# Performance work log

Hardware: AMD Instinct MI355X
Metric: run time of the kernel (lower is better)

The kernel has to match this reference:

```python
import jax, jax.numpy as jnp
import numpy as np

N = 50000      # nodes
E = 1600000    # edges (avg degree 32)
DIN, DH, DOUT = 256, 128, 64


def gcn_conv(x, W, b, row, col, w, n):
    """One GCNConv layer (self-loops already appended to row/col/w).
    row = source nodes, col = target nodes; aggregate at targets."""
    xw = x @ W                                        # [n, d_out]
    deg = jax.ops.segment_sum(w, col, num_segments=n)  # in-degree weighted
    dinv = jnp.where(deg > 0, jax.lax.rsqrt(deg), 0.0)
    norm = dinv[row] * w * dinv[col]                  # [E+n]
    msg = norm[:, None] * xw[row]                     # [E+n, d_out] gather
    out = jax.ops.segment_sum(msg, col, num_segments=n)
    return out + b


def setup_inputs() -> dict:
    key = jax.random.key(0)
    k = jax.random.split(key, 6)
    x = jax.random.normal(k[0], (N, DIN), dtype=jnp.float32)
    edge_index = jax.random.randint(k[1], (2, E), 0, N)
    edge_weight = jax.random.uniform(k[2], (E,), dtype=jnp.float32)
    W1 = jax.random.normal(k[3], (DIN, DH), dtype=jnp.float32) * (1.0 / np.sqrt(DIN))
    b1 = jnp.zeros((DH,), dtype=jnp.float32)
    W2 = jax.random.normal(k[4], (DH, DOUT), dtype=jnp.float32) * (1.0 / np.sqrt(DH))
    b2 = jnp.zeros((DOUT,), dtype=jnp.float32)
    return {"x": x, "edge_index": edge_index, "edge_weight": edge_weight,
            "W1": W1, "b1": b1, "W2": W2, "b2": b2}


def reference(x, edge_index, edge_weight, W1, b1, W2, b2):
    n = x.shape[0]
    loops = jnp.arange(n, dtype=edge_index.dtype)
    row = jnp.concatenate([edge_index[0], loops])
    col = jnp.concatenate([edge_index[1], loops])
    w = jnp.concatenate([edge_weight, jnp.ones((n,), dtype=edge_weight.dtype)])
    h = gcn_conv(x, W1, b1, row, col, w, n)
    h = jax.nn.relu(h)
    # dropout(p=0.2) is identity in eval mode
    h = gcn_conv(h, W2, b2, row, col, w, n)
    return jax.nn.log_softmax(h, axis=-1)
```

## Files before the change

### kernel.cpp

```cpp
#include <hip/hip_runtime.h>
#include <hip/hip_bf16.h>
#include <cstddef>


#define DIN 256
#define DH  128
#define DOUT 64
#define NPB 100
#define NBMAX 512

typedef __bf16 bf16x8 __attribute__((ext_vector_type(8)));
typedef float f32x4 __attribute__((ext_vector_type(4)));

__device__ __forceinline__ float bflo(unsigned u) { return __uint_as_float(u << 16); }
__device__ __forceinline__ float bfhi(unsigned u) { return __uint_as_float(u & 0xffff0000u); }
__device__ __forceinline__ unsigned short f2bf(float f) {
    unsigned u = __float_as_uint(f);
    unsigned r = (u + 0x7fffu + ((u >> 16) & 1u)) >> 16;
    return (unsigned short)r;
}

__device__ __forceinline__ int2 ldrec(const int2* __restrict__ e, int idx, int last, int fb) {
    int ci = idx < last ? idx : last;
    int2 r = e[ci];
    if (idx > last) { r.x = fb; r.y = 0; }
    return r;
}

__global__ void prep_w_kernel(const float* __restrict__ W1, const float* __restrict__ W2,
                              unsigned short* __restrict__ wt1, unsigned short* __restrict__ wt2) {
    int i = blockIdx.x * 256 + threadIdx.x;
    if (i < DH * DIN) {
        int nn = i >> 8, k = i & 255;
        wt1[i] = f2bf(W1[k * DH + nn]);
    } else {
        int j = i - DH * DIN;
        if (j < DOUT * DH) {
            int nn = j >> 7, k = j & 127;
            wt2[j] = f2bf(W2[k * DOUT + nn]);
        }
    }
}

__launch_bounds__(256)
__global__ void hist_kernel(const int* __restrict__ col, int* __restrict__ bh,
                            int E, int Ec, int NB) {
    __shared__ int hist[NBMAX];
    int p = blockIdx.x, t = threadIdx.x;
    for (int b = t; b < NB; b += 256) hist[b] = 0;
    __syncthreads();
    int s = p * Ec, e = min(s + Ec, E);
    for (int i = s + t; i < e; i += 256) atomicAdd(&hist[col[i] / NPB], 1);
    __syncthreads();
    for (int b = t; b < NB; b += 256) bh[p * NB + b] = hist[b];
}

__launch_bounds__(512)
__global__ void colscan_kernel(int* __restrict__ bh, int* __restrict__ btotal,
                               int P, int NB) {
    __shared__ int arr[512];
    int b = blockIdx.x, t = threadIdx.x;
    arr[t] = (t < P) ? bh[t * NB + b] : 0;
    __syncthreads();
    for (int off = 1; off < 512; off <<= 1) {
        int v = (t >= off) ? arr[t - off] : 0;
        __syncthreads();
        arr[t] += v;
        __syncthreads();
    }
    int excl = (t == 0) ? 0 : arr[t - 1];
    if (t < P) bh[t * NB + b] = excl;
    if (t == P - 1) btotal[b] = arr[t];
}

__launch_bounds__(512)
__global__ void basescan_kernel(const int* __restrict__ btotal, int* __restrict__ bbase,
                                int* __restrict__ rowptr, int NB, int n, int E) {
    __shared__ int arr[512];
    int t = threadIdx.x;
    arr[t] = (t < NB) ? btotal[t] : 0;
    __syncthreads();
    for (int off = 1; off < 512; off <<= 1) {
        int v = (t >= off) ? arr[t - off] : 0;
        __syncthreads();
        arr[t] += v;
        __syncthreads();
    }
    int excl = (t == 0) ? 0 : arr[t - 1];
    if (t <= NB) bbase[t] = excl;
    if (t == 511) rowptr[n] = E;
}

__launch_bounds__(256)
__global__ void scatter_kernel(const int* __restrict__ row, const int* __restrict__ col,
                               const float* __restrict__ w, const int* __restrict__ bh,
                               const int* __restrict__ bbase, int2* __restrict__ part,
                               int E, int Ec, int NB) {
    __shared__ int cur[NBMAX];
    int p = blockIdx.x, t = threadIdx.x;
    for (int b = t; b < NB; b += 256) cur[b] = bbase[b] + bh[p * NB + b];
    __syncthreads();
    int s = p * Ec, e = min(s + Ec, E);
    for (int i = s + t; i < e; i += 256) {
        int c = col[i];
        int r = row[i];
        int b = c / NPB;
        int pos = atomicAdd(&cur[b], 1);
        part[pos] = make_int2(r | ((c - b * NPB) << 16), __float_as_int(w[i]));
    }
}

__launch_bounds__(256)
__global__ void bucket_csr_kernel(const int2* __restrict__ part, const int* __restrict__ bbase,
                                  float* __restrict__ dinv, int* __restrict__ rowptr,
                                  int2* __restrict__ final_e, int n) {
    __shared__ int   hist[NPB];
    __shared__ float wsum[NPB];
    __shared__ int   nbase[NPB];
    __shared__ int   cur[NPB];
    int b = blockIdx.x, t = threadIdx.x;
    if (t < NPB) { hist[t] = 0; wsum[t] = 0.0f; }
    __syncthreads();
    int s = bbase[b], e = bbase[b + 1];
    for (int i = s + t; i < e; i += 256) {
        int2 rec = part[i];
        int cl = rec.x >> 16;
        atomicAdd(&hist[cl], 1);
        atomicAdd(&wsum[cl], __int_as_float(rec.y));
    }
    __syncthreads();
    if (t == 0) {
        int run = 0;
        for (int k = 0; k < NPB; ++k) { nbase[k] = run; run += hist[k]; }
    }
    __syncthreads();
    if (t < NPB) {
        int node = b * NPB + t;
        if (node < n) {
            dinv[node] = rsqrtf(1.0f + wsum[t]);
            rowptr[node] = s + nbase[t];
        }
        cur[t] = nbase[t];
    }
    __syncthreads();
    for (int i = s + t; i < e; i += 256) {
        int2 rec = part[i];
        int cl = rec.x >> 16;
        int q = s + atomicAdd(&cur[cl], 1);
        final_e[q] = make_int2(rec.x & 0xffff, rec.y);
    }
}

template <int K, int M>
__launch_bounds__(256)
__global__ void gemm_mfma_kernel(const float* __restrict__ A,
                                 const unsigned short* __restrict__ Wt,
                                 const float* __restrict__ scale,
                                 unsigned short* __restrict__ C, int N) {
    constexpr int BK = 64, LD = BK + 8;
    constexpr int WN = M / 4;
    constexpr int NT = WN / 16;
    constexpr int CLD = M + 8;
    constexpr int SM = (64 * LD + M * LD) > (64 * CLD) ? (64 * LD + M * LD) : (64 * CLD);
    __shared__ unsigned short smem[SM];
    __shared__ float sdv[64];
    unsigned short* As = smem;
    unsigned short* Bs = smem + 64 * LD;

    const int tid = threadIdx.x;
    const int row0 = blockIdx.x * 64;
    const int lane = tid & 63;
    const int quad = lane >> 4, r16 = lane & 15;
    const int n0 = (tid >> 6) * WN;

    if (tid < 64) {
        int r = row0 + tid;
        sdv[tid] = (r < N) ? scale[r] : 0.0f;
    }

    f32x4 acc[4][NT];
#pragma unroll
    for (int mt = 0; mt < 4; ++mt)
#pragma unroll
        for (int nt = 0; nt < NT; ++nt)
            acc[mt][nt] = (f32x4){0.f, 0.f, 0.f, 0.f};

    for (int k0 = 0; k0 < K; k0 += BK) {
#pragma unroll
        for (int j = 0; j < 4; ++j) {
            int idx = tid + j * 256;
            int m = idx >> 4;
            int q = idx & 15;
            int gr = row0 + m;
            float4 v = make_float4(0.f, 0.f, 0.f, 0.f);
            if (gr < N) v = *(const float4*)&A[(size_t)gr * K + k0 + q * 4];
            ushort4 s4;
            s4.x = f2bf(v.x); s4.y = f2bf(v.y); s4.z = f2bf(v.z); s4.w = f2bf(v.w);
            *(ushort4*)&As[m * LD + q * 4] = s4;
        }
#pragma unroll
        for (int j = 0; j < M * 8 / 256; ++j) {
            int idx = tid + j * 256;
            int nn = idx >> 3;
            int q = idx & 7;
            uint4 v = *(const uint4*)&Wt[(size_t)nn * K + k0 + q * 8];
            *(uint4*)&Bs[nn * LD + q * 8] = v;
        }
        __syncthreads();
#pragma unroll
        for (int ks = 0; ks < BK / 32; ++ks) {
            bf16x8 af[4], bfr[NT];
#pragma unroll
            for (int nt = 0; nt < NT; ++nt)
                bfr[nt] = *(const bf16x8*)&Bs[(n0 + nt * 16 + r16) * LD + ks * 32 + quad * 8];
#pragma unroll
            for (int mt = 0; mt < 4; ++mt)
                af[mt] = *(const bf16x8*)&As[(mt * 16 + r16) * LD + ks * 32 + quad * 8];
#pragma unroll
            for (int mt = 0; mt < 4; ++mt)
#pragma unroll
                for (int nt = 0; nt < NT; ++nt)
                    acc[mt][nt] = __builtin_amdgcn_mfma_f32_16x16x32_bf16(
                        af[mt], bfr[nt], acc[mt][nt], 0, 0, 0);
        }
        __syncthreads();
    }
    unsigned short* Cs = smem;
#pragma unroll
    for (int mt = 0; mt < 4; ++mt) {
#pragma unroll
        for (int i = 0; i < 4; ++i) {
            int r = mt * 16 + quad * 4 + i;
            float sc = sdv[r];
#pragma unroll
            for (int nt = 0; nt < NT; ++nt)
                Cs[r * CLD + n0 + nt * 16 + r16] = f2bf(acc[mt][nt][i] * sc);
        }
    }
    __syncthreads();
#pragma unroll
    for (int j = 0; j < 64 * M / 8 / 256; ++j) {
        int idx = tid + j * 256;
        int r = idx / (M / 8);
        int q = idx % (M / 8);
        int gr = row0 + r;
        if (gr < N) {
            uint4 v = *(const uint4*)&Cs[r * CLD + q * 8];
            *(uint4*)&C[(size_t)gr * M + q * 8] = v;
        }
    }
}

#define ACC8(v, wgt)                                            \
    a0 += (wgt) * bflo((v).x); a1 += (wgt) * bfhi((v).x);       \
    a2 += (wgt) * bflo((v).y); a3 += (wgt) * bfhi((v).y);       \
    a4 += (wgt) * bflo((v).z); a5 += (wgt) * bfhi((v).z);       \
    a6 += (wgt) * bflo((v).w); a7 += (wgt) * bfhi((v).w);

__launch_bounds__(256, 8)
__global__ void agg1_kernel(const unsigned short* __restrict__ xw,
                            const int* __restrict__ rowptr,
                            const int2* __restrict__ edge,
                            const float* __restrict__ dinv,
                            const float* __restrict__ bias,
                            float* __restrict__ out, int n) {
    int node = blockIdx.x * 4 + (threadIdx.x >> 6);
    if (node >= n) return;
    int lane = threadIdx.x & 63;
    int qw = lane >> 4, sub = lane & 15;
    const char* xb = (const char*)xw;
    const unsigned ssub = (unsigned)sub << 4;
    float di = dinv[node];

    float a0 = 0.f, a1 = 0.f, a2 = 0.f, a3 = 0.f;
    float a4 = 0.f, a5 = 0.f, a6 = 0.f, a7 = 0.f;
    if (qw == 0) {
        uint4 u = *(const uint4*)(xb + (((unsigned)node) << 8) + ssub);
        a0 = bflo(u.x); a1 = bfhi(u.x); a2 = bflo(u.y); a3 = bfhi(u.y);
        a4 = bflo(u.z); a5 = bfhi(u.z); a6 = bflo(u.w); a7 = bfhi(u.w);
    }

    int p = rowptr[node], p1 = rowptr[node + 1];
    int sbase = 4 * qw;
    int2 ea, eb, ec, ed;
    bool have = (p + 16 <= p1);
    if (have) {
        const int2* rp = edge + p + sbase;
        ea = rp[0]; eb = rp[1]; ec = rp[2]; ed = rp[3];
    }
#pragma unroll 1
    while (have) {
        uint4 v0 = *(const uint4*)(xb + (((unsigned)ea.x) << 8) + ssub);
        uint4 v1 = *(const uint4*)(xb + (((unsigned)eb.x) << 8) + ssub);
        uint4 v2 = *(const uint4*)(xb + (((unsigned)ec.x) << 8) + ssub);
        uint4 v3 = *(const uint4*)(xb + (((unsigned)ed.x) << 8) + ssub);
        float w0 = __int_as_float(ea.y), w1 = __int_as_float(eb.y);
        float w2 = __int_as_float(ec.y), w3 = __int_as_float(ed.y);
        p += 16;
        have = (p + 16 <= p1);
        if (have) {
            const int2* rp = edge + p + sbase;
            ea = rp[0]; eb = rp[1]; ec = rp[2]; ed = rp[3];
        }
        ACC8(v0, w0); ACC8(v1, w1); ACC8(v2, w2); ACC8(v3, w3);
    }
    int rem = p1 - p;
    if (rem > 0) {
        int last = p1 - 1, b2 = p + sbase;
        int2 e0 = ldrec(edge, b2, last, node);
        int2 e1 = ldrec(edge, b2 + 1, last, node);
        int2 e2 = ldrec(edge, b2 + 2, last, node);
        int2 e3 = ldrec(edge, b2 + 3, last, node);
        uint4 v0 = *(const uint4*)(xb + (((unsigned)e0.x) << 8) + ssub);
        uint4 v1 = *(const uint4*)(xb + (((unsigned)e1.x) << 8) + ssub);
        uint4 v2 = *(const uint4*)(xb + (((unsigned)e2.x) << 8) + ssub);
        uint4 v3 = *(const uint4*)(xb + (((unsigned)e3.x) << 8) + ssub);
        float w0 = __int_as_float(e0.y), w1 = __int_as_float(e1.y);
        float w2 = __int_as_float(e2.y), w3 = __int_as_float(e3.y);
        ACC8(v0, w0); ACC8(v1, w1); ACC8(v2, w2); ACC8(v3, w3);
    }
    a0 += __shfl_xor(a0, 16); a0 += __shfl_xor(a0, 32);
    a1 += __shfl_xor(a1, 16); a1 += __shfl_xor(a1, 32);
    a2 += __shfl_xor(a2, 16); a2 += __shfl_xor(a2, 32);
    a3 += __shfl_xor(a3, 16); a3 += __shfl_xor(a3, 32);
    a4 += __shfl_xor(a4, 16); a4 += __shfl_xor(a4, 32);
    a5 += __shfl_xor(a5, 16); a5 += __shfl_xor(a5, 32);
    a6 += __shfl_xor(a6, 16); a6 += __shfl_xor(a6, 32);
    a7 += __shfl_xor(a7, 16); a7 += __shfl_xor(a7, 32);
    if (qw < 2) {
        float4 b = ((const float4*)bias)[2 * sub + qw];
        float4 o = (qw == 0) ? make_float4(a0, a1, a2, a3)
                             : make_float4(a4, a5, a6, a7);
        o.x = fmaxf(di * o.x + b.x, 0.f);
        o.y = fmaxf(di * o.y + b.y, 0.f);
        o.z = fmaxf(di * o.z + b.z, 0.f);
        o.w = fmaxf(di * o.w + b.w, 0.f);
        ((float4*)out)[(size_t)node * 32 + 2 * sub + qw] = o;
    }
}

__launch_bounds__(256, 8)
__global__ void agg2_kernel(const unsigned short* __restrict__ xw,
                            const int* __restrict__ rowptr,
                            const int2* __restrict__ edge,
                            const float* __restrict__ dinv,
                            const float* __restrict__ bias,
                            float* __restrict__ out, int n) {
    int node = blockIdx.x * 4 + (threadIdx.x >> 6);
    if (node >= n) return;
    int lane = threadIdx.x & 63;
    int oct = lane >> 3, sub = lane & 7;
    const char* xb = (const char*)xw;
    const unsigned ssub = (unsigned)sub << 4;
    float di = dinv[node];

    float a0 = 0.f, a1 = 0.f, a2 = 0.f, a3 = 0.f;
    float a4 = 0.f, a5 = 0.f, a6 = 0.f, a7 = 0.f;
    if (oct == 0) {
        uint4 u = *(const uint4*)(xb + (((unsigned)node) << 7) + ssub);
        a0 = bflo(u.x); a1 = bfhi(u.x); a2 = bflo(u.y); a3 = bfhi(u.y);
        a4 = bflo(u.z); a5 = bfhi(u.z); a6 = bflo(u.w); a7 = bfhi(u.w);
    }

    int p = rowptr[node], p1 = rowptr[node + 1];
    int sbase = 4 * oct;
    int2 ea, eb, ec, ed;
    bool have = (p + 32 <= p1);
    if (have) {
        const int2* rp = edge + p + sbase;
        ea = rp[0]; eb = rp[1]; ec = rp[2]; ed = rp[3];
    }
#pragma unroll 1
    while (have) {
        uint4 v0 = *(const uint4*)(xb + (((unsigned)ea.x) << 7) + ssub);
        uint4 v1 = *(const uint4*)(xb + (((unsigned)eb.x) << 7) + ssub);
        uint4 v2 = *(const uint4*)(xb + (((unsigned)ec.x) << 7) + ssub);
        uint4 v3 = *(const uint4*)(xb + (((unsigned)ed.x) << 7) + ssub);
        float w0 = __int_as_float(ea.y), w1 = __int_as_float(eb.y);
        float w2 = __int_as_float(ec.y), w3 = __int_as_float(ed.y);
        p += 32;
        have = (p + 32 <= p1);
        if (have) {
            const int2* rp = edge + p + sbase;
            ea = rp[0]; eb = rp[1]; ec = rp[2]; ed = rp[3];
        }
        ACC8(v0, w0); ACC8(v1, w1); ACC8(v2, w2); ACC8(v3, w3);
    }
    int rem = p1 - p;
    if (rem > 0) {
        int last = p1 - 1, b2 = p + sbase;
        int2 e0 = ldrec(edge, b2, last, node);
        int2 e1 = ldrec(edge, b2 + 1, last, node);
        int2 e2 = ldrec(edge, b2 + 2, last, node);
        int2 e3 = ldrec(edge, b2 + 3, last, node);
        uint4 v0 = *(const uint4*)(xb + (((unsigned)e0.x) << 7) + ssub);
        uint4 v1 = *(const uint4*)(xb + (((unsigned)e1.x) << 7) + ssub);
        uint4 v2 = *(const uint4*)(xb + (((unsigned)e2.x) << 7) + ssub);
        uint4 v3 = *(const uint4*)(xb + (((unsigned)e3.x) << 7) + ssub);
        float w0 = __int_as_float(e0.y), w1 = __int_as_float(e1.y);
        float w2 = __int_as_float(e2.y), w3 = __int_as_float(e3.y);
        ACC8(v0, w0); ACC8(v1, w1); ACC8(v2, w2); ACC8(v3, w3);
    }
    a0 += __shfl_xor(a0, 8); a0 += __shfl_xor(a0, 16); a0 += __shfl_xor(a0, 32);
    a1 += __shfl_xor(a1, 8); a1 += __shfl_xor(a1, 16); a1 += __shfl_xor(a1, 32);
    a2 += __shfl_xor(a2, 8); a2 += __shfl_xor(a2, 16); a2 += __shfl_xor(a2, 32);
    a3 += __shfl_xor(a3, 8); a3 += __shfl_xor(a3, 16); a3 += __shfl_xor(a3, 32);
    a4 += __shfl_xor(a4, 8); a4 += __shfl_xor(a4, 16); a4 += __shfl_xor(a4, 32);
    a5 += __shfl_xor(a5, 8); a5 += __shfl_xor(a5, 16); a5 += __shfl_xor(a5, 32);
    a6 += __shfl_xor(a6, 8); a6 += __shfl_xor(a6, 16); a6 += __shfl_xor(a6, 32);
    a7 += __shfl_xor(a7, 8); a7 += __shfl_xor(a7, 16); a7 += __shfl_xor(a7, 32);
    const float4* bp = (const float4*)bias;
    float4 bl = bp[2 * sub], bh = bp[2 * sub + 1];
    a0 = di * a0 + bl.x; a1 = di * a1 + bl.y; a2 = di * a2 + bl.z; a3 = di * a3 + bl.w;
    a4 = di * a4 + bh.x; a5 = di * a5 + bh.y; a6 = di * a6 + bh.z; a7 = di * a7 + bh.w;
    float m = fmaxf(fmaxf(fmaxf(a0, a1), fmaxf(a2, a3)),
                    fmaxf(fmaxf(a4, a5), fmaxf(a6, a7)));
    m = fmaxf(m, __shfl_xor(m, 4));
    m = fmaxf(m, __shfl_xor(m, 2));
    m = fmaxf(m, __shfl_xor(m, 1));
    float s = __expf(a0 - m) + __expf(a1 - m) + __expf(a2 - m) + __expf(a3 - m)
            + __expf(a4 - m) + __expf(a5 - m) + __expf(a6 - m) + __expf(a7 - m);
    s += __shfl_xor(s, 4);
    s += __shfl_xor(s, 2);
    s += __shfl_xor(s, 1);
    float lse = m + __logf(s);
    if (oct < 2) {
        float4 o = (oct == 0) ? make_float4(a0, a1, a2, a3)
                              : make_float4(a4, a5, a6, a7);
        ((float4*)out)[(size_t)node * 16 + 2 * sub + oct] =
            make_float4(o.x - lse, o.y - lse, o.z - lse, o.w - lse);
    }
}

extern "C" void kernel_launch(void* const* d_in, const int* in_sizes, int n_in,
                              void* d_out, int out_size, void* d_ws, size_t ws_size,
                              hipStream_t stream) {
    const float* x  = (const float*)d_in[0];
    const int*   ei = (const int*)d_in[1];
    const float* ew = (const float*)d_in[2];
    const float* W1 = (const float*)d_in[3];
    const float* b1 = (const float*)d_in[4];
    const float* W2 = (const float*)d_in[5];
    const float* b2 = (const float*)d_in[6];
    float* out = (float*)d_out;

    const int n = in_sizes[0] / DIN;
    const int E = in_sizes[2];
    const int* row = ei;
    const int* col = ei + E;

    const int NB = (n + NPB - 1) / NPB;
    const int P  = NB;
    const int Ec = (E + P - 1) / P;

    char* ptr = (char*)d_ws;
    auto alloc = [&](size_t bytes) -> void* {
        void* r = (void*)ptr;
        ptr += (bytes + 255) & ~(size_t)255;
        return r;
    };
    int*   bh     = (int*)  alloc((size_t)P * NB * 4);
    int*   btotal = (int*)  alloc((size_t)NB * 4);
    int*   bbase  = (int*)  alloc((size_t)(NB + 1) * 4);
    int*   rowptr = (int*)  alloc((size_t)(n + 1) * 4);
    float* dinv   = (float*)alloc((size_t)n * 4);
    int2*  edge   = (int2*) alloc((size_t)E * 8);
    unsigned short* xw1 = (unsigned short*)alloc((size_t)n * DH * 2);
    unsigned short* wt1 = (unsigned short*)alloc((size_t)DH * DIN * 2);
    unsigned short* wt2 = (unsigned short*)alloc((size_t)DOUT * DH * 2);
    char* tail = (char*)alloc((size_t)n * DH * 4);
    int2*  part = (int2*)tail;
    float* h1   = (float*)tail;
    unsigned short* xw2 = xw1;

    const int nb_g = (n + 63) / 64;
    const int nb_a = (n + 3) / 4;

    prep_w_kernel<<<(DH * DIN + DOUT * DH + 255) / 256, 256, 0, stream>>>(W1, W2, wt1, wt2);
    hist_kernel<<<P, 256, 0, stream>>>(col, bh, E, Ec, NB);
    colscan_kernel<<<NB, 512, 0, stream>>>(bh, btotal, P, NB);
    basescan_kernel<<<1, 512, 0, stream>>>(btotal, bbase, rowptr, NB, n, E);
    scatter_kernel<<<P, 256, 0, stream>>>(row, col, ew, bh, bbase, part, E, Ec, NB);
    bucket_csr_kernel<<<NB, 256, 0, stream>>>(part, bbase, dinv, rowptr, edge, n);

    gemm_mfma_kernel<DIN, DH><<<nb_g, 256, 0, stream>>>(x, wt1, dinv, xw1, n);
    agg1_kernel<<<nb_a, 256, 0, stream>>>(xw1, rowptr, edge, dinv, b1, h1, n);
    gemm_mfma_kernel<DH, DOUT><<<nb_g, 256, 0, stream>>>(h1, wt2, dinv, xw2, n);
    agg2_kernel<<<nb_a, 256, 0, stream>>>(xw2, rowptr, edge, dinv, b2, out, n);
}
```

Baseline: 282.5 us.

## Pack CSR edges into 32-bit records with fp16 weights and software-pipeline gathers

Edge records drop from int2 (row index plus fp32 weight) to one 32-bit word holding a 16-bit source index and an fp16 weight, halving edge-list traffic in both aggregation kernels. The aggregation loops now issue the next batch's feature gathers before accumulating the current one, overlapping gather latency with math at the cost of more registers; launch bounds are lowered to 6 blocks to make room. Output writes and edge loads use nontemporal hints. The fp16 weight adds rounding error, and the 16-bit index only holds for node counts up to 65536.

```diff
diff --git a/kernel.cpp b/kernel.cpp
--- a/kernel.cpp
+++ b/kernel.cpp
@@ -1,5 +1,6 @@
 #include <hip/hip_runtime.h>
 #include <hip/hip_bf16.h>
+#include <hip/hip_fp16.h>
 #include <cstddef>
 
 
@@ -19,12 +20,8 @@
     unsigned r = (u + 0x7fffu + ((u >> 16) & 1u)) >> 16;
     return (unsigned short)r;
 }
-
-__device__ __forceinline__ int2 ldrec(const int2* __restrict__ e, int idx, int last, int fb) {
-    int ci = idx < last ? idx : last;
-    int2 r = e[ci];
-    if (idx > last) { r.x = fb; r.y = 0; }
-    return r;
+__device__ __forceinline__ float wdec(unsigned rec) {
+    return __half2float(__ushort_as_half((unsigned short)(rec >> 16)));
 }
 
 __global__ void prep_w_kernel(const float* __restrict__ W1, const float* __restrict__ W2,
@@ -113,7 +110,7 @@
 __launch_bounds__(256)
 __global__ void bucket_csr_kernel(const int2* __restrict__ part, const int* __restrict__ bbase,
                                   float* __restrict__ dinv, int* __restrict__ rowptr,
-                                  int2* __restrict__ final_e, int n) {
+                                  unsigned* __restrict__ final_e, int n) {
     __shared__ int   hist[NPB];
     __shared__ float wsum[NPB];
     __shared__ int   nbase[NPB];
@@ -147,7 +144,8 @@
         int2 rec = part[i];
         int cl = rec.x >> 16;
         int q = s + atomicAdd(&cur[cl], 1);
-        final_e[q] = make_int2(rec.x & 0xffff, rec.y);
+        unsigned short ws = __half_as_ushort(__float2half_rn(__int_as_float(rec.y)));
+        final_e[q] = ((unsigned)rec.x & 0xffffu) | ((unsigned)ws << 16);
     }
 }
 
@@ -257,10 +255,10 @@
     a4 += (wgt) * bflo((v).z); a5 += (wgt) * bfhi((v).z);       \
     a6 += (wgt) * bflo((v).w); a7 += (wgt) * bfhi((v).w);
 
-__launch_bounds__(256, 8)
+__launch_bounds__(256, 6)
 __global__ void agg1_kernel(const unsigned short* __restrict__ xw,
                             const int* __restrict__ rowptr,
-                            const int2* __restrict__ edge,
+                            const unsigned* __restrict__ edge,
                             const float* __restrict__ dinv,
                             const float* __restrict__ bias,
                             float* __restrict__ out, int n) {
@@ -281,43 +279,58 @@
     }
 
     int p = rowptr[node], p1 = rowptr[node + 1];
-    int sbase = 4 * qw;
-    int2 ea, eb, ec, ed;
+    int sb = 4 * qw;
+    unsigned r0, r1, r2, r3;
+    uint4 v0, v1, v2, v3;
     bool have = (p + 16 <= p1);
     if (have) {
-        const int2* rp = edge + p + sbase;
-        ea = rp[0]; eb = rp[1]; ec = rp[2]; ed = rp[3];
+        const unsigned* rp = edge + p + sb;
+        r0 = __builtin_nontemporal_load(rp);
+        r1 = __builtin_nontemporal_load(rp + 1);
+        r2 = __builtin_nontemporal_load(rp + 2);
+        r3 = __builtin_nontemporal_load(rp + 3);
+        v0 = *(const uint4*)(xb + ((r0 & 0xffffu) << 8) + ssub);
+        v1 = *(const uint4*)(xb + ((r1 & 0xffffu) << 8) + ssub);
+        v2 = *(const uint4*)(xb + ((r2 & 0xffffu) << 8) + ssub);
+        v3 = *(const uint4*)(xb + ((r3 & 0xffffu) << 8) + ssub);
     }
 #pragma unroll 1
     while (have) {
-        uint4 v0 = *(const uint4*)(xb + (((unsigned)ea.x) << 8) + ssub);
-        uint4 v1 = *(const uint4*)(xb + (((unsigned)eb.x) << 8) + ssub);
-        uint4 v2 = *(const uint4*)(xb + (((unsigned)ec.x) << 8) + ssub);
-        uint4 v3 = *(const uint4*)(xb + (((unsigned)ed.x) << 8) + ssub);
-        float w0 = __int_as_float(ea.y), w1 = __int_as_float(eb.y);
-        float w2 = __int_as_float(ec.y), w3 = __int_as_float(ed.y);
         p += 16;
-        have = (p + 16 <= p1);
-        if (have) {
-            const int2* rp = edge + p + sbase;
-            ea = rp[0]; eb = rp[1]; ec = rp[2]; ed = rp[3];
-        }
+        bool havn = (p + 16 <= p1);
+        unsigned m0 = 0, m1 = 0, m2 = 0, m3 = 0;
+        uint4 u0 = {0,0,0,0}, u1 = {0,0,0,0}, u2 = {0,0,0,0}, u3 = {0,0,0,0};
+        if (havn) {
+            const unsigned* rp = edge + p + sb;
+            m0 = __builtin_nontemporal_load(rp);
+            m1 = __builtin_nontemporal_load(rp + 1);
+            m2 = __builtin_nontemporal_load(rp + 2);
+            m3 = __builtin_nontemporal_load(rp + 3);
+            u0 = *(const uint4*)(xb + ((m0 & 0xffffu) << 8) + ssub);
+            u1 = *(const uint4*)(xb + ((m1 & 0xffffu) << 8) + ssub);
+            u2 = *(const uint4*)(xb + ((m2 & 0xffffu) << 8) + ssub);
+            u3 = *(const uint4*)(xb + ((m3 & 0xffffu) << 8) + ssub);
+        }
+        float w0 = wdec(r0), w1 = wdec(r1), w2 = wdec(r2), w3 = wdec(r3);
         ACC8(v0, w0); ACC8(v1, w1); ACC8(v2, w2); ACC8(v3, w3);
+        r0 = m0; r1 = m1; r2 = m2; r3 = m3;
+        v0 = u0; v1 = u1; v2 = u2; v3 = u3;
+        have = havn;
     }
     int rem = p1 - p;
     if (rem > 0) {
-        int last = p1 - 1, b2 = p + sbase;
-        int2 e0 = ldrec(edge, b2, last, node);
-        int2 e1 = ldrec(edge, b2 + 1, last, node);
-        int2 e2 = ldrec(edge, b2 + 2, last, node);
-        int2 e3 = ldrec(edge, b2 + 3, last, node);
-        uint4 v0 = *(const uint4*)(xb + (((unsigned)e0.x) << 8) + ssub);
-        uint4 v1 = *(const uint4*)(xb + (((unsigned)e1.x) << 8) + ssub);
-        uint4 v2 = *(const uint4*)(xb + (((unsigned)e2.x) << 8) + ssub);
-        uint4 v3 = *(const uint4*)(xb + (((unsigned)e3.x) << 8) + ssub);
-        float w0 = __int_as_float(e0.y), w1 = __int_as_float(e1.y);
-        float w2 = __int_as_float(e2.y), w3 = __int_as_float(e3.y);
-        ACC8(v0, w0); ACC8(v1, w1); ACC8(v2, w2); ACC8(v3, w3);
+        int last = p1 - 1, b = p + sb;
+        unsigned e0 = edge[min(b, last)],     e1 = edge[min(b + 1, last)];
+        unsigned e2 = edge[min(b + 2, last)], e3 = edge[min(b + 3, last)];
+        float w0 = (b     <= last) ? wdec(e0) : 0.f;
+        float w1 = (b + 1 <= last) ? wdec(e1) : 0.f;
+        float w2 = (b + 2 <= last) ? wdec(e2) : 0.f;
+        float w3 = (b + 3 <= last) ? wdec(e3) : 0.f;
+        uint4 t0 = *(const uint4*)(xb + ((e0 & 0xffffu) << 8) + ssub);
+        uint4 t1 = *(const uint4*)(xb + ((e1 & 0xffffu) << 8) + ssub);
+        uint4 t2 = *(const uint4*)(xb + ((e2 & 0xffffu) << 8) + ssub);
+        uint4 t3 = *(const uint4*)(xb + ((e3 & 0xffffu) << 8) + ssub);
+        ACC8(t0, w0); ACC8(t1, w1); ACC8(t2, w2); ACC8(t3, w3);
     }
     a0 += __shfl_xor(a0, 16); a0 += __shfl_xor(a0, 32);
     a1 += __shfl_xor(a1, 16); a1 += __shfl_xor(a1, 32);
@@ -329,20 +342,21 @@
     a7 += __shfl_xor(a7, 16); a7 += __shfl_xor(a7, 32);
     if (qw < 2) {
         float4 b = ((const float4*)bias)[2 * sub + qw];
-        float4 o = (qw == 0) ? make_float4(a0, a1, a2, a3)
-                             : make_float4(a4, a5, a6, a7);
+        f32x4 o;
+        if (qw == 0) { o.x = a0; o.y = a1; o.z = a2; o.w = a3; }
+        else         { o.x = a4; o.y = a5; o.z = a6; o.w = a7; }
         o.x = fmaxf(di * o.x + b.x, 0.f);
         o.y = fmaxf(di * o.y + b.y, 0.f);
         o.z = fmaxf(di * o.z + b.z, 0.f);
         o.w = fmaxf(di * o.w + b.w, 0.f);
-        ((float4*)out)[(size_t)node * 32 + 2 * sub + qw] = o;
-    }
-}
-
-__launch_bounds__(256, 8)
+        __builtin_nontemporal_store(o, (f32x4*)out + (size_t)node * 32 + 2 * sub + qw);
+    }
+}
+
+__launch_bounds__(256, 6)
 __global__ void agg2_kernel(const unsigned short* __restrict__ xw,
                             const int* __restrict__ rowptr,
-                            const int2* __restrict__ edge,
+                            const unsigned* __restrict__ edge,
                             const float* __restrict__ dinv,
                             const float* __restrict__ bias,
                             float* __restrict__ out, int n) {
@@ -363,43 +377,58 @@
     }
 
     int p = rowptr[node], p1 = rowptr[node + 1];
-    int sbase = 4 * oct;
-    int2 ea, eb, ec, ed;
+    int sb = 4 * oct;
+    unsigned r0, r1, r2, r3;
+    uint4 v0, v1, v2, v3;
     bool have = (p + 32 <= p1);
     if (have) {
-        const int2* rp = edge + p + sbase;
-        ea = rp[0]; eb = rp[1]; ec = rp[2]; ed = rp[3];
+        const unsigned* rp = edge + p + sb;
+        r0 = __builtin_nontemporal_load(rp);
+        r1 = __builtin_nontemporal_load(rp + 1);
+        r2 = __builtin_nontemporal_load(rp + 2);
+        r3 = __builtin_nontemporal_load(rp + 3);
+        v0 = *(const uint4*)(xb + ((r0 & 0xffffu) << 7) + ssub);
+        v1 = *(const uint4*)(xb + ((r1 & 0xffffu) << 7) + ssub);
+        v2 = *(const uint4*)(xb + ((r2 & 0xffffu) << 7) + ssub);
+        v3 = *(const uint4*)(xb + ((r3 & 0xffffu) << 7) + ssub);
     }
 #pragma unroll 1
     while (have) {
-        uint4 v0 = *(const uint4*)(xb + (((unsigned)ea.x) << 7) + ssub);
-        uint4 v1 = *(const uint4*)(xb + (((unsigned)eb.x) << 7) + ssub);
-        uint4 v2 = *(const uint4*)(xb + (((unsigned)ec.x) << 7) + ssub);
-        uint4 v3 = *(const uint4*)(xb + (((unsigned)ed.x) << 7) + ssub);
-        float w0 = __int_as_float(ea.y), w1 = __int_as_float(eb.y);
-        float w2 = __int_as_float(ec.y), w3 = __int_as_float(ed.y);
         p += 32;
-        have = (p + 32 <= p1);
-        if (have) {
-            const int2* rp = edge + p + sbase;
-            ea = rp[0]; eb = rp[1]; ec = rp[2]; ed = rp[3];
-        }
+        bool havn = (p + 32 <= p1);
+        unsigned m0 = 0, m1 = 0, m2 = 0, m3 = 0;
+        uint4 u0 = {0,0,0,0}, u1 = {0,0,0,0}, u2 = {0,0,0,0}, u3 = {0,0,0,0};
+        if (havn) {
+            const unsigned* rp = edge + p + sb;
+            m0 = __builtin_nontemporal_load(rp);
+            m1 = __builtin_nontemporal_load(rp + 1);
+            m2 = __builtin_nontemporal_load(rp + 2);
+            m3 = __builtin_nontemporal_load(rp + 3);
+            u0 = *(const uint4*)(xb + ((m0 & 0xffffu) << 7) + ssub);
+            u1 = *(const uint4*)(xb + ((m1 & 0xffffu) << 7) + ssub);
+            u2 = *(const uint4*)(xb + ((m2 & 0xffffu) << 7) + ssub);
+            u3 = *(const uint4*)(xb + ((m3 & 0xffffu) << 7) + ssub);
+        }
+        float w0 = wdec(r0), w1 = wdec(r1), w2 = wdec(r2), w3 = wdec(r3);
         ACC8(v0, w0); ACC8(v1, w1); ACC8(v2, w2); ACC8(v3, w3);
+        r0 = m0; r1 = m1; r2 = m2; r3 = m3;
+        v0 = u0; v1 = u1; v2 = u2; v3 = u3;
+        have = havn;
     }
     int rem = p1 - p;
     if (rem > 0) {
-        int last = p1 - 1, b2 = p + sbase;
-        int2 e0 = ldrec(edge, b2, last, node);
-        int2 e1 = ldrec(edge, b2 + 1, last, node);
-        int2 e2 = ldrec(edge, b2 + 2, last, node);
-        int2 e3 = ldrec(edge, b2 + 3, last, node);
-        uint4 v0 = *(const uint4*)(xb + (((unsigned)e0.x) << 7) + ssub);
-        uint4 v1 = *(const uint4*)(xb + (((unsigned)e1.x) << 7) + ssub);
-        uint4 v2 = *(const uint4*)(xb + (((unsigned)e2.x) << 7) + ssub);
-        uint4 v3 = *(const uint4*)(xb + (((unsigned)e3.x) << 7) + ssub);
-        float w0 = __int_as_float(e0.y), w1 = __int_as_float(e1.y);
-        float w2 = __int_as_float(e2.y), w3 = __int_as_float(e3.y);
-        ACC8(v0, w0); ACC8(v1, w1); ACC8(v2, w2); ACC8(v3, w3);
+        int last = p1 - 1, b = p + sb;
+        unsigned e0 = edge[min(b, last)],     e1 = edge[min(b + 1, last)];
+        unsigned e2 = edge[min(b + 2, last)], e3 = edge[min(b + 3, last)];
+        float w0 = (b     <= last) ? wdec(e0) : 0.f;
+        float w1 = (b + 1 <= last) ? wdec(e1) : 0.f;
+        float w2 = (b + 2 <= last) ? wdec(e2) : 0.f;
+        float w3 = (b + 3 <= last) ? wdec(e3) : 0.f;
+        uint4 t0 = *(const uint4*)(xb + ((e0 & 0xffffu) << 7) + ssub);
+        uint4 t1 = *(const uint4*)(xb + ((e1 & 0xffffu) << 7) + ssub);
+        uint4 t2 = *(const uint4*)(xb + ((e2 & 0xffffu) << 7) + ssub);
+        uint4 t3 = *(const uint4*)(xb + ((e3 & 0xffffu) << 7) + ssub);
+        ACC8(t0, w0); ACC8(t1, w1); ACC8(t2, w2); ACC8(t3, w3);
     }
     a0 += __shfl_xor(a0, 8); a0 += __shfl_xor(a0, 16); a0 += __shfl_xor(a0, 32);
     a1 += __shfl_xor(a1, 8); a1 += __shfl_xor(a1, 16); a1 += __shfl_xor(a1, 32);
@@ -425,10 +454,10 @@
     s += __shfl_xor(s, 1);
     float lse = m + __logf(s);
     if (oct < 2) {
-        float4 o = (oct == 0) ? make_float4(a0, a1, a2, a3)
-                              : make_float4(a4, a5, a6, a7);
-        ((float4*)out)[(size_t)node * 16 + 2 * sub + oct] =
-            make_float4(o.x - lse, o.y - lse, o.z - lse, o.w - lse);
+        f32x4 o;
+        if (oct == 0) { o.x = a0 - lse; o.y = a1 - lse; o.z = a2 - lse; o.w = a3 - lse; }
+        else          { o.x = a4 - lse; o.y = a5 - lse; o.z = a6 - lse; o.w = a7 - lse; }
+        __builtin_nontemporal_store(o, (f32x4*)out + (size_t)node * 16 + 2 * sub + oct);
     }
 }
 
@@ -464,7 +493,7 @@
     int*   bbase  = (int*)  alloc((size_t)(NB + 1) * 4);
     int*   rowptr = (int*)  alloc((size_t)(n + 1) * 4);
     float* dinv   = (float*)alloc((size_t)n * 4);
-    int2*  edge   = (int2*) alloc((size_t)E * 8);
+    unsigned* edge = (unsigned*)alloc((size_t)E * 4);
     unsigned short* xw1 = (unsigned short*)alloc((size_t)n * DH * 2);
     unsigned short* wt1 = (unsigned short*)alloc((size_t)DH * DIN * 2);
     unsigned short* wt2 = (unsigned short*)alloc((size_t)DOUT * DH * 2);
```

Measured after the change: 276.1 us. 2.3% less time.
